# Kernel tuning notes

Hardware: AMD Instinct MI355X
Metric: run time of the kernel (lower is better)

Reference implementation:

```python
import jax, jax.numpy as jnp
import numpy as np

TAU = 1.0
TOP_K = 2
TOP_C = 8
EPS = 1e-12


def _stable_softmax(v):
    # matches torch: exp(v - max) / (sum + 1e-12)
    e = jnp.exp(v - jnp.max(v, axis=-1, keepdims=True))
    return e / (jnp.sum(e, axis=-1, keepdims=True) + EPS)


def setup_inputs() -> dict:
    key = jax.random.key(0)
    kx, kw = jax.random.split(key)
    B, D, M = 16384, 2048, 64
    x = jax.random.normal(kx, (B, D), dtype=jnp.float32)
    W = jax.random.normal(kw, (M, D), dtype=jnp.float32) * (1.0 / np.sqrt(D))
    return {"x": x, "W": W}


def reference(x, W):
    # router GEMM: [B, D] x [M, D]^T -> [B, M]
    router_logits = jnp.einsum('bd,md->bm', x, W)
    scaled_logits = router_logits / TAU
    probs = _stable_softmax(scaled_logits)
    # double top-k: first candidates (top_c), then top_k among candidates
    topc_vals, topc_idx = jax.lax.top_k(scaled_logits, TOP_C)   # [B, C]
    topk_vals, topk_pos_in_C = jax.lax.top_k(topc_vals, TOP_K)  # [B, K]
    topk_idx = jnp.take_along_axis(topc_idx, topk_pos_in_C, axis=1)
    topk_weights = _stable_softmax(topk_vals)
    return (topk_idx.astype(jnp.int64), topk_weights, probs, topc_idx.astype(jnp.int64))
```

## Files before the change

kernel.cpp:

```cpp
#include <hip/hip_runtime.h>


typedef __attribute__((ext_vector_type(8))) short short8;
typedef __attribute__((ext_vector_type(4))) float f32x4;

constexpr int Bq = 16384;
constexpr int Dk = 2048;
constexpr int Me = 64;
constexpr int WAVES = 8;
constexpr int ROWS = 32;
constexpr int KCHUNK = Dk / WAVES;
constexpr int NT = KCHUNK / 32;

constexpr size_t OFF_TOPK_IDX = 0;
constexpr size_t OFF_TOPK_W   = (size_t)Bq * 2;
constexpr size_t OFF_PROBS    = (size_t)Bq * 4;
constexpr size_t OFF_TOPC_IDX = (size_t)Bq * 4 + (size_t)Bq * 64;

__device__ __forceinline__ unsigned f2bf2(float lo, float hi) {
  unsigned r;
  asm("v_cvt_pk_bf16_f32 %0, %1, %2" : "=v"(r) : "v"(lo), "v"(hi));
  return r;
}
__device__ __forceinline__ float bflo(unsigned u) { return __builtin_bit_cast(float, u << 16); }
__device__ __forceinline__ float bfhi(unsigned u) { return __builtin_bit_cast(float, u & 0xFFFF0000u); }

__device__ __forceinline__ void split3(const float af[8], short8& s0, short8& s1, short8& s2) {
  uint4 q0, q1, q2;
  unsigned* p0 = &q0.x; unsigned* p1 = &q1.x; unsigned* p2 = &q2.x;
  #pragma unroll
  for (int p = 0; p < 4; ++p) {
    float a = af[2 * p], b = af[2 * p + 1];
    unsigned c0 = f2bf2(a, b);
    float r0a = a - bflo(c0), r0b = b - bfhi(c0);
    unsigned c1 = f2bf2(r0a, r0b);
    float r1a = r0a - bflo(c1), r1b = r0b - bfhi(c1);
    unsigned c2 = f2bf2(r1a, r1b);
    p0[p] = c0; p1[p] = c1; p2[p] = c2;
  }
  s0 = __builtin_bit_cast(short8, q0);
  s1 = __builtin_bit_cast(short8, q1);
  s2 = __builtin_bit_cast(short8, q2);
}

__global__ void wsplit_kernel(const float* __restrict__ W,
                              unsigned short* __restrict__ w0,
                              unsigned short* __restrict__ w1,
                              unsigned short* __restrict__ w2) {
  int t = blockIdx.x * blockDim.x + threadIdx.x;
  int kt = t >> 8, n = (t >> 6) & 3, L = t & 63;
  int e  = n * 16 + (L & 15);
  int kb = kt * 32 + ((L >> 4) << 3);
  const float* src = W + (size_t)e * Dk + kb;
  float4 a = *reinterpret_cast<const float4*>(src);
  float4 b = *reinterpret_cast<const float4*>(src + 4);
  float af[8] = {a.x, a.y, a.z, a.w, b.x, b.y, b.z, b.w};
  short8 s0, s1, s2;
  split3(af, s0, s1, s2);
  *reinterpret_cast<short8*>(w0 + (size_t)t * 8) = s0;
  *reinterpret_cast<short8*>(w1 + (size_t)t * 8) = s1;
  *reinterpret_cast<short8*>(w2 + (size_t)t * 8) = s2;
}

__global__ __launch_bounds__(512, 4)
void gating_mfma(const float* __restrict__ x,
                 const unsigned short* __restrict__ w0,
                 const unsigned short* __restrict__ w1,
                 const unsigned short* __restrict__ w2,
                 float* __restrict__ out) {
  __shared__ __align__(16) char smem[WAVES * ROWS * 64 * 4];
  typedef float XaT[ROWS][36];
  XaT* xa = reinterpret_cast<XaT*>(smem);
  typedef float PartT[ROWS][64];
  PartT* part = reinterpret_cast<PartT*>(smem);

  const int tid  = threadIdx.x;
  const int wv   = tid >> 6;
  const int L    = tid & 63;
  const int lidx = L & 15;
  const int kgrp = L >> 4;
  const int rowBase = blockIdx.x * ROWS;
  const int kBase = wv * KCHUNK;

  const int srow = L >> 3;
  const int sc4  = (L & 7) << 2;
  const float* xg0 = x + (size_t)(rowBase +      srow) * Dk + kBase + sc4;
  const float* xg1 = x + (size_t)(rowBase +  8 + srow) * Dk + kBase + sc4;
  const float* xg2 = x + (size_t)(rowBase + 16 + srow) * Dk + kBase + sc4;
  const float* xg3 = x + (size_t)(rowBase + 24 + srow) * Dk + kBase + sc4;

  const size_t bbase = (size_t)kBase * 64 + (size_t)L * 8;

  f32x4 acc[2][4];
  #pragma unroll
  for (int rg = 0; rg < 2; ++rg)
    #pragma unroll
    for (int n = 0; n < 4; ++n) acc[rg][n] = (f32x4){0.f, 0.f, 0.f, 0.f};

  *reinterpret_cast<float4*>(&xa[wv][     srow][sc4]) = *reinterpret_cast<const float4*>(xg0);
  *reinterpret_cast<float4*>(&xa[wv][ 8 + srow][sc4]) = *reinterpret_cast<const float4*>(xg1);
  *reinterpret_cast<float4*>(&xa[wv][16 + srow][sc4]) = *reinterpret_cast<const float4*>(xg2);
  *reinterpret_cast<float4*>(&xa[wv][24 + srow][sc4]) = *reinterpret_cast<const float4*>(xg3);

  #pragma unroll 1
  for (int kt = 0; kt < NT; ++kt) {
    float4 aLo0 = *reinterpret_cast<const float4*>(&xa[wv][     lidx][kgrp * 8]);
    float4 aHi0 = *reinterpret_cast<const float4*>(&xa[wv][     lidx][kgrp * 8 + 4]);
    float4 aLo1 = *reinterpret_cast<const float4*>(&xa[wv][16 + lidx][kgrp * 8]);
    float4 aHi1 = *reinterpret_cast<const float4*>(&xa[wv][16 + lidx][kgrp * 8 + 4]);

    float4 h0, h1, h2, h3;
    if (kt < NT - 1) {
      h0 = *reinterpret_cast<const float4*>(xg0 + (kt + 1) * 32);
      h1 = *reinterpret_cast<const float4*>(xg1 + (kt + 1) * 32);
      h2 = *reinterpret_cast<const float4*>(xg2 + (kt + 1) * 32);
      h3 = *reinterpret_cast<const float4*>(xg3 + (kt + 1) * 32);
    }

    const size_t to = bbase + (size_t)kt * 2048;

    short8 b0[4];
    #pragma unroll
    for (int n = 0; n < 4; ++n) b0[n] = *reinterpret_cast<const short8*>(w0 + to + n * 512);

    float af0[8] = {aLo0.x, aLo0.y, aLo0.z, aLo0.w, aHi0.x, aHi0.y, aHi0.z, aHi0.w};
    float af1[8] = {aLo1.x, aLo1.y, aLo1.z, aLo1.w, aHi1.x, aHi1.y, aHi1.z, aHi1.w};
    short8 xs00, xs10, xs20, xs01, xs11, xs21;
    split3(af0, xs00, xs10, xs20);
    split3(af1, xs01, xs11, xs21);

    short8 b1[4];
    #pragma unroll
    for (int n = 0; n < 4; ++n) b1[n] = *reinterpret_cast<const short8*>(w1 + to + n * 512);

    #pragma unroll
    for (int n = 0; n < 4; ++n) acc[0][n] = __builtin_amdgcn_mfma_f32_16x16x32_bf16(xs00, b0[n], acc[0][n], 0, 0, 0);
    #pragma unroll
    for (int n = 0; n < 4; ++n) acc[1][n] = __builtin_amdgcn_mfma_f32_16x16x32_bf16(xs01, b0[n], acc[1][n], 0, 0, 0);
    #pragma unroll
    for (int n = 0; n < 4; ++n) acc[0][n] = __builtin_amdgcn_mfma_f32_16x16x32_bf16(xs10, b0[n], acc[0][n], 0, 0, 0);
    #pragma unroll
    for (int n = 0; n < 4; ++n) acc[1][n] = __builtin_amdgcn_mfma_f32_16x16x32_bf16(xs11, b0[n], acc[1][n], 0, 0, 0);
    #pragma unroll
    for (int n = 0; n < 4; ++n) acc[0][n] = __builtin_amdgcn_mfma_f32_16x16x32_bf16(xs20, b0[n], acc[0][n], 0, 0, 0);
    #pragma unroll
    for (int n = 0; n < 4; ++n) acc[1][n] = __builtin_amdgcn_mfma_f32_16x16x32_bf16(xs21, b0[n], acc[1][n], 0, 0, 0);

    short8 b2[4];
    #pragma unroll
    for (int n = 0; n < 4; ++n) b2[n] = *reinterpret_cast<const short8*>(w2 + to + n * 512);

    #pragma unroll
    for (int n = 0; n < 4; ++n) acc[0][n] = __builtin_amdgcn_mfma_f32_16x16x32_bf16(xs00, b1[n], acc[0][n], 0, 0, 0);
    #pragma unroll
    for (int n = 0; n < 4; ++n) acc[1][n] = __builtin_amdgcn_mfma_f32_16x16x32_bf16(xs01, b1[n], acc[1][n], 0, 0, 0);
    #pragma unroll
    for (int n = 0; n < 4; ++n) acc[0][n] = __builtin_amdgcn_mfma_f32_16x16x32_bf16(xs10, b1[n], acc[0][n], 0, 0, 0);
    #pragma unroll
    for (int n = 0; n < 4; ++n) acc[1][n] = __builtin_amdgcn_mfma_f32_16x16x32_bf16(xs11, b1[n], acc[1][n], 0, 0, 0);

    #pragma unroll
    for (int n = 0; n < 4; ++n) acc[0][n] = __builtin_amdgcn_mfma_f32_16x16x32_bf16(xs00, b2[n], acc[0][n], 0, 0, 0);
    #pragma unroll
    for (int n = 0; n < 4; ++n) acc[1][n] = __builtin_amdgcn_mfma_f32_16x16x32_bf16(xs01, b2[n], acc[1][n], 0, 0, 0);

    if (kt < NT - 1) {
      *reinterpret_cast<float4*>(&xa[wv][     srow][sc4]) = h0;
      *reinterpret_cast<float4*>(&xa[wv][ 8 + srow][sc4]) = h1;
      *reinterpret_cast<float4*>(&xa[wv][16 + srow][sc4]) = h2;
      *reinterpret_cast<float4*>(&xa[wv][24 + srow][sc4]) = h3;
    }
  }

  __syncthreads();

  #pragma unroll
  for (int rg = 0; rg < 2; ++rg)
    #pragma unroll
    for (int n = 0; n < 4; ++n)
      #pragma unroll
      for (int r = 0; r < 4; ++r)
        part[wv][rg * 16 + kgrp * 4 + r][n * 16 + lidx] = acc[rg][n][r];
  __syncthreads();

  const int row = tid >> 4;
  const int g   = tid & 15;
  const int c4  = g * 4;
  const size_t grow = (size_t)rowBase + row;

  float4 v = {0.f, 0.f, 0.f, 0.f};
  #pragma unroll
  for (int p = 0; p < WAVES; ++p) {
    float4 t = *reinterpret_cast<const float4*>(&part[p][row][c4]);
    v.x += t.x; v.y += t.y; v.z += t.z; v.w += t.w;
  }
  float pv[4] = {v.x, v.y, v.z, v.w};

  float mx = fmaxf(fmaxf(pv[0], pv[1]), fmaxf(pv[2], pv[3]));
  #pragma unroll
  for (int m = 1; m < 16; m <<= 1) mx = fmaxf(mx, __shfl_xor(mx, m));
  float e[4], sum = 0.f;
  #pragma unroll
  for (int j = 0; j < 4; ++j) { e[j] = expf(pv[j] - mx); sum += e[j]; }
  #pragma unroll
  for (int m = 1; m < 16; m <<= 1) sum += __shfl_xor(sum, m);
  const float inv = 1.f / (sum + 1e-12f);
  float4 pw = {e[0] * inv, e[1] * inv, e[2] * inv, e[3] * inv};
  *reinterpret_cast<float4*>(out + OFF_PROBS + grow * 64 + c4) = pw;

  unsigned taken = 0;
  int bidx0 = 0, bidx1 = 0;
  float tv0 = 0.f, tv1 = 0.f;
  #pragma unroll 1
  for (int rank = 0; rank < 8; ++rank) {
    float best = -3.4e38f;
    int bl = -1;
    #pragma unroll
    for (int j = 0; j < 4; ++j)
      if (!((taken >> j) & 1u) && pv[j] > best) { best = pv[j]; bl = j; }
    int bidx = (bl >= 0) ? (c4 + bl) : (1 << 30);
    #pragma unroll
    for (int m = 1; m < 16; m <<= 1) {
      float ov = __shfl_xor(best, m);
      int   oi = __shfl_xor(bidx, m);
      if (ov > best || (ov == best && oi < bidx)) { best = ov; bidx = oi; }
    }
    if (bidx >= c4 && bidx < c4 + 4) taken |= 1u << (bidx - c4);
    if (g == 0) out[OFF_TOPC_IDX + grow * 8 + rank] = (float)bidx;
    if (rank == 0) { tv0 = best; bidx0 = bidx; }
    if (rank == 1) { tv1 = best; bidx1 = bidx; }
  }

  if (g == 0) {
    out[OFF_TOPK_IDX + grow * 2 + 0] = (float)bidx0;
    out[OFF_TOPK_IDX + grow * 2 + 1] = (float)bidx1;
    const float e1  = expf(tv1 - tv0);
    const float den = 1.f + e1 + 1e-12f;
    out[OFF_TOPK_W + grow * 2 + 0] = 1.f / den;
    out[OFF_TOPK_W + grow * 2 + 1] = e1 / den;
  }
}

extern "C" void kernel_launch(void* const* d_in, const int* in_sizes, int n_in,
                              void* d_out, int out_size, void* d_ws, size_t ws_size,
                              hipStream_t stream) {
  const float* x = (const float*)d_in[0];
  const float* W = (const float*)d_in[1];
  float* out = (float*)d_out;

  unsigned short* w0 = (unsigned short*)d_ws;
  unsigned short* w1 = w0 + (size_t)Me * Dk;
  unsigned short* w2 = w1 + (size_t)Me * Dk;

  hipLaunchKernelGGL(wsplit_kernel, dim3((Me * Dk / 8) / 256), dim3(256), 0, stream, W, w0, w1, w2);
  hipLaunchKernelGGL(gating_mfma, dim3(Bq / ROWS), dim3(512), 0, stream, x, w0, w1, w2, out);
}
```

Baseline: 46.43 us.

## Stage x tiles via direct global-to-LDS loads with double buffering and XOR swizzle

Replaces the register-staged x tile copy with __builtin_amdgcn_global_load_lds into a double-buffered per-wave LDS region. An XOR swizzle on the global column replaces the padded row layout to avoid bank conflicts. All three W split loads are also hoisted to the top of each iteration. The aim is to cut VGPR pressure and the register round trip, and to overlap the next tile's fetch with the MFMA work. The risk is correctness: the loop has no explicit vmcnt wait or barrier before reading the staged LDS, so it relies on the compiler inserting waits. Hoisting the W loads also raises live registers.

```diff
diff --git a/kernel.cpp b/kernel.cpp
--- a/kernel.cpp
+++ b/kernel.cpp
@@ -68,8 +68,8 @@
                  const unsigned short* __restrict__ w1,
                  const unsigned short* __restrict__ w2,
                  float* __restrict__ out) {
-  __shared__ __align__(16) char smem[WAVES * ROWS * 64 * 4];
-  typedef float XaT[ROWS][36];
+  __shared__ __align__(16) float smem[2 * WAVES * ROWS * 32];
+  typedef float XaT[ROWS][32];
   XaT* xa = reinterpret_cast<XaT*>(smem);
   typedef float PartT[ROWS][64];
   PartT* part = reinterpret_cast<PartT*>(smem);
@@ -83,13 +83,14 @@
   const int kBase = wv * KCHUNK;
 
   const int srow = L >> 3;
-  const int sc4  = (L & 7) << 2;
-  const float* xg0 = x + (size_t)(rowBase +      srow) * Dk + kBase + sc4;
-  const float* xg1 = x + (size_t)(rowBase +  8 + srow) * Dk + kBase + sc4;
-  const float* xg2 = x + (size_t)(rowBase + 16 + srow) * Dk + kBase + sc4;
-  const float* xg3 = x + (size_t)(rowBase + 24 + srow) * Dk + kBase + sc4;
+  const int scol = ((L & 7) ^ (srow & 7)) << 2;
+  const float* xg0 = x + (size_t)(rowBase +      srow) * Dk + kBase + scol;
+  const float* xg1 = x + (size_t)(rowBase +  8 + srow) * Dk + kBase + scol;
+  const float* xg2 = x + (size_t)(rowBase + 16 + srow) * Dk + kBase + scol;
+  const float* xg3 = x + (size_t)(rowBase + 24 + srow) * Dk + kBase + scol;
 
   const size_t bbase = (size_t)kBase * 64 + (size_t)L * 8;
+  const int s = L & 7;
 
   f32x4 acc[2][4];
   #pragma unroll
@@ -97,31 +98,46 @@
     #pragma unroll
     for (int n = 0; n < 4; ++n) acc[rg][n] = (f32x4){0.f, 0.f, 0.f, 0.f};
 
-  *reinterpret_cast<float4*>(&xa[wv][     srow][sc4]) = *reinterpret_cast<const float4*>(xg0);
-  *reinterpret_cast<float4*>(&xa[wv][ 8 + srow][sc4]) = *reinterpret_cast<const float4*>(xg1);
-  *reinterpret_cast<float4*>(&xa[wv][16 + srow][sc4]) = *reinterpret_cast<const float4*>(xg2);
-  *reinterpret_cast<float4*>(&xa[wv][24 + srow][sc4]) = *reinterpret_cast<const float4*>(xg3);
+  auto stage = [&](int buf, int kt_) {
+    float* lb = &xa[buf * WAVES + wv][0][0];
+    const int o = kt_ * 32;
+    __builtin_amdgcn_global_load_lds(
+        (const __attribute__((address_space(1))) void*)(xg0 + o),
+        (__attribute__((address_space(3))) void*)(lb),             16, 0, 0);
+    __builtin_amdgcn_global_load_lds(
+        (const __attribute__((address_space(1))) void*)(xg1 + o),
+        (__attribute__((address_space(3))) void*)(lb + 8 * 32),    16, 0, 0);
+    __builtin_amdgcn_global_load_lds(
+        (const __attribute__((address_space(1))) void*)(xg2 + o),
+        (__attribute__((address_space(3))) void*)(lb + 16 * 32),   16, 0, 0);
+    __builtin_amdgcn_global_load_lds(
+        (const __attribute__((address_space(1))) void*)(xg3 + o),
+        (__attribute__((address_space(3))) void*)(lb + 24 * 32),   16, 0, 0);
+  };
+
+  stage(0, 0);
 
   #pragma unroll 1
   for (int kt = 0; kt < NT; ++kt) {
-    float4 aLo0 = *reinterpret_cast<const float4*>(&xa[wv][     lidx][kgrp * 8]);
-    float4 aHi0 = *reinterpret_cast<const float4*>(&xa[wv][     lidx][kgrp * 8 + 4]);
-    float4 aLo1 = *reinterpret_cast<const float4*>(&xa[wv][16 + lidx][kgrp * 8]);
-    float4 aHi1 = *reinterpret_cast<const float4*>(&xa[wv][16 + lidx][kgrp * 8 + 4]);
-
-    float4 h0, h1, h2, h3;
-    if (kt < NT - 1) {
-      h0 = *reinterpret_cast<const float4*>(xg0 + (kt + 1) * 32);
-      h1 = *reinterpret_cast<const float4*>(xg1 + (kt + 1) * 32);
-      h2 = *reinterpret_cast<const float4*>(xg2 + (kt + 1) * 32);
-      h3 = *reinterpret_cast<const float4*>(xg3 + (kt + 1) * 32);
-    }
-
     const size_t to = bbase + (size_t)kt * 2048;
 
-    short8 b0[4];
+    short8 b0[4], b1[4], b2[4];
     #pragma unroll
     for (int n = 0; n < 4; ++n) b0[n] = *reinterpret_cast<const short8*>(w0 + to + n * 512);
+    #pragma unroll
+    for (int n = 0; n < 4; ++n) b1[n] = *reinterpret_cast<const short8*>(w1 + to + n * 512);
+    #pragma unroll
+    for (int n = 0; n < 4; ++n) b2[n] = *reinterpret_cast<const short8*>(w2 + to + n * 512);
+
+    if (kt + 1 < NT) stage((kt + 1) & 1, kt + 1);
+
+    const int xb = (kt & 1) * WAVES + wv;
+    const int u0 = (((2 * kgrp)     ^ s) << 2);
+    const int u1 = (((2 * kgrp + 1) ^ s) << 2);
+    float4 aLo0 = *reinterpret_cast<const float4*>(&xa[xb][     lidx][u0]);
+    float4 aHi0 = *reinterpret_cast<const float4*>(&xa[xb][     lidx][u1]);
+    float4 aLo1 = *reinterpret_cast<const float4*>(&xa[xb][16 + lidx][u0]);
+    float4 aHi1 = *reinterpret_cast<const float4*>(&xa[xb][16 + lidx][u1]);
 
     float af0[8] = {aLo0.x, aLo0.y, aLo0.z, aLo0.w, aHi0.x, aHi0.y, aHi0.z, aHi0.w};
     float af1[8] = {aLo1.x, aLo1.y, aLo1.z, aLo1.w, aHi1.x, aHi1.y, aHi1.z, aHi1.w};
@@ -129,10 +145,6 @@
     split3(af0, xs00, xs10, xs20);
     split3(af1, xs01, xs11, xs21);
 
-    short8 b1[4];
-    #pragma unroll
-    for (int n = 0; n < 4; ++n) b1[n] = *reinterpret_cast<const short8*>(w1 + to + n * 512);
-
     #pragma unroll
     for (int n = 0; n < 4; ++n) acc[0][n] = __builtin_amdgcn_mfma_f32_16x16x32_bf16(xs00, b0[n], acc[0][n], 0, 0, 0);
     #pragma unroll
@@ -146,10 +158,6 @@
     #pragma unroll
     for (int n = 0; n < 4; ++n) acc[1][n] = __builtin_amdgcn_mfma_f32_16x16x32_bf16(xs21, b0[n], acc[1][n], 0, 0, 0);
 
-    short8 b2[4];
-    #pragma unroll
-    for (int n = 0; n < 4; ++n) b2[n] = *reinterpret_cast<const short8*>(w2 + to + n * 512);
-
     #pragma unroll
     for (int n = 0; n < 4; ++n) acc[0][n] = __builtin_amdgcn_mfma_f32_16x16x32_bf16(xs00, b1[n], acc[0][n], 0, 0, 0);
     #pragma unroll
@@ -163,13 +171,6 @@
     for (int n = 0; n < 4; ++n) acc[0][n] = __builtin_amdgcn_mfma_f32_16x16x32_bf16(xs00, b2[n], acc[0][n], 0, 0, 0);
     #pragma unroll
     for (int n = 0; n < 4; ++n) acc[1][n] = __builtin_amdgcn_mfma_f32_16x16x32_bf16(xs01, b2[n], acc[1][n], 0, 0, 0);
-
-    if (kt < NT - 1) {
-      *reinterpret_cast<float4*>(&xa[wv][     srow][sc4]) = h0;
-      *reinterpret_cast<float4*>(&xa[wv][ 8 + srow][sc4]) = h1;
-      *reinterpret_cast<float4*>(&xa[wv][16 + srow][sc4]) = h2;
-      *reinterpret_cast<float4*>(&xa[wv][24 + srow][sc4]) = h3;
-    }
   }
 
   __syncthreads();
```

Result: slower. 47.45 us (+2.2%).

## Double-buffer x tile in LDS with XOR swizzle and software-pipelined bf16 split

Applied to the files above, without the earlier changes.

Restructures the per-wave K loop into a two-stage pipeline. The x tile is double-buffered in LDS with an XOR-swizzled layout, global loads run two steps ahead, and the bf16 three-way split for the next step is computed before the current step's MFMAs, with a sched_barrier separating the phases. The loop is also fully unrolled, and all weight fragments are loaded up front. The intent is to hide LDS and global latency behind MFMA work and to avoid bank conflicts, at the cost of more VGPRs, which may reduce occupancy under launch_bounds(512,4).

```diff
diff --git a/kernel.cpp b/kernel.cpp
--- a/kernel.cpp
+++ b/kernel.cpp
@@ -68,9 +68,7 @@
                  const unsigned short* __restrict__ w1,
                  const unsigned short* __restrict__ w2,
                  float* __restrict__ out) {
-  __shared__ __align__(16) char smem[WAVES * ROWS * 64 * 4];
-  typedef float XaT[ROWS][36];
-  XaT* xa = reinterpret_cast<XaT*>(smem);
+  __shared__ __align__(16) float smem[2 * WAVES * ROWS * 32];
   typedef float PartT[ROWS][64];
   PartT* part = reinterpret_cast<PartT*>(smem);
 
@@ -89,6 +87,13 @@
   const float* xg2 = x + (size_t)(rowBase + 16 + srow) * Dk + kBase + sc4;
   const float* xg3 = x + (size_t)(rowBase + 24 + srow) * Dk + kBase + sc4;
 
+  float* tile0 = smem + (size_t)wv * (ROWS * 32);
+  float* tile1 = smem + (size_t)(WAVES + wv) * (ROWS * 32);
+  const int uW = ((L & 7) ^ (srow & 7)) << 2;
+  const int s7 = lidx & 7;
+  const int uR0 = (((2 * kgrp)     ^ s7) << 2);
+  const int uR1 = (((2 * kgrp + 1) ^ s7) << 2);
+
   const size_t bbase = (size_t)kBase * 64 + (size_t)L * 8;
 
   f32x4 acc[2][4];
@@ -97,79 +102,98 @@
     #pragma unroll
     for (int n = 0; n < 4; ++n) acc[rg][n] = (f32x4){0.f, 0.f, 0.f, 0.f};
 
-  *reinterpret_cast<float4*>(&xa[wv][     srow][sc4]) = *reinterpret_cast<const float4*>(xg0);
-  *reinterpret_cast<float4*>(&xa[wv][ 8 + srow][sc4]) = *reinterpret_cast<const float4*>(xg1);
-  *reinterpret_cast<float4*>(&xa[wv][16 + srow][sc4]) = *reinterpret_cast<const float4*>(xg2);
-  *reinterpret_cast<float4*>(&xa[wv][24 + srow][sc4]) = *reinterpret_cast<const float4*>(xg3);
-
-  #pragma unroll 1
+  short8 xs[2][6];
+
+  float4 h0 = *reinterpret_cast<const float4*>(xg0);
+  float4 h1 = *reinterpret_cast<const float4*>(xg1);
+  float4 h2 = *reinterpret_cast<const float4*>(xg2);
+  float4 h3 = *reinterpret_cast<const float4*>(xg3);
+  *reinterpret_cast<float4*>(tile0 + (     srow) * 32 + uW) = h0;
+  *reinterpret_cast<float4*>(tile0 + ( 8 + srow) * 32 + uW) = h1;
+  *reinterpret_cast<float4*>(tile0 + (16 + srow) * 32 + uW) = h2;
+  *reinterpret_cast<float4*>(tile0 + (24 + srow) * 32 + uW) = h3;
+  h0 = *reinterpret_cast<const float4*>(xg0 + 32);
+  h1 = *reinterpret_cast<const float4*>(xg1 + 32);
+  h2 = *reinterpret_cast<const float4*>(xg2 + 32);
+  h3 = *reinterpret_cast<const float4*>(xg3 + 32);
+  {
+    float4 r0 = *reinterpret_cast<const float4*>(tile0 + (     lidx) * 32 + uR0);
+    float4 r1 = *reinterpret_cast<const float4*>(tile0 + (     lidx) * 32 + uR1);
+    float4 r2 = *reinterpret_cast<const float4*>(tile0 + (16 + lidx) * 32 + uR0);
+    float4 r3 = *reinterpret_cast<const float4*>(tile0 + (16 + lidx) * 32 + uR1);
+    float af0[8] = {r0.x, r0.y, r0.z, r0.w, r1.x, r1.y, r1.z, r1.w};
+    float af1[8] = {r2.x, r2.y, r2.z, r2.w, r3.x, r3.y, r3.z, r3.w};
+    split3(af0, xs[0][0], xs[0][1], xs[0][2]);
+    split3(af1, xs[0][3], xs[0][4], xs[0][5]);
+  }
+
+  #pragma unroll
   for (int kt = 0; kt < NT; ++kt) {
-    float4 aLo0 = *reinterpret_cast<const float4*>(&xa[wv][     lidx][kgrp * 8]);
-    float4 aHi0 = *reinterpret_cast<const float4*>(&xa[wv][     lidx][kgrp * 8 + 4]);
-    float4 aLo1 = *reinterpret_cast<const float4*>(&xa[wv][16 + lidx][kgrp * 8]);
-    float4 aHi1 = *reinterpret_cast<const float4*>(&xa[wv][16 + lidx][kgrp * 8 + 4]);
-
-    float4 h0, h1, h2, h3;
-    if (kt < NT - 1) {
-      h0 = *reinterpret_cast<const float4*>(xg0 + (kt + 1) * 32);
-      h1 = *reinterpret_cast<const float4*>(xg1 + (kt + 1) * 32);
-      h2 = *reinterpret_cast<const float4*>(xg2 + (kt + 1) * 32);
-      h3 = *reinterpret_cast<const float4*>(xg3 + (kt + 1) * 32);
+    const int p = kt & 1, q = p ^ 1;
+    const size_t to = bbase + (size_t)kt * 2048;
+
+    short8 b0[4], b1[4], b2[4];
+    #pragma unroll
+    for (int n = 0; n < 4; ++n) b0[n] = *reinterpret_cast<const short8*>(w0 + to + n * 512);
+    #pragma unroll
+    for (int n = 0; n < 4; ++n) b1[n] = *reinterpret_cast<const short8*>(w1 + to + n * 512);
+    #pragma unroll
+    for (int n = 0; n < 4; ++n) b2[n] = *reinterpret_cast<const short8*>(w2 + to + n * 512);
+
+    float4 r0, r1, r2, r3;
+    if (kt + 1 < NT) {
+      float* wb = ((kt + 1) & 1) ? tile1 : tile0;
+      *reinterpret_cast<float4*>(wb + (     srow) * 32 + uW) = h0;
+      *reinterpret_cast<float4*>(wb + ( 8 + srow) * 32 + uW) = h1;
+      *reinterpret_cast<float4*>(wb + (16 + srow) * 32 + uW) = h2;
+      *reinterpret_cast<float4*>(wb + (24 + srow) * 32 + uW) = h3;
+      if (kt + 2 < NT) {
+        h0 = *reinterpret_cast<const float4*>(xg0 + (kt + 2) * 32);
+        h1 = *reinterpret_cast<const float4*>(xg1 + (kt + 2) * 32);
+        h2 = *reinterpret_cast<const float4*>(xg2 + (kt + 2) * 32);
+        h3 = *reinterpret_cast<const float4*>(xg3 + (kt + 2) * 32);
+      }
+      r0 = *reinterpret_cast<const float4*>(wb + (     lidx) * 32 + uR0);
+      r1 = *reinterpret_cast<const float4*>(wb + (     lidx) * 32 + uR1);
+      r2 = *reinterpret_cast<const float4*>(wb + (16 + lidx) * 32 + uR0);
+      r3 = *reinterpret_cast<const float4*>(wb + (16 + lidx) * 32 + uR1);
     }
 
-    const size_t to = bbase + (size_t)kt * 2048;
-
-    short8 b0[4];
-    #pragma unroll
-    for (int n = 0; n < 4; ++n) b0[n] = *reinterpret_cast<const short8*>(w0 + to + n * 512);
-
-    float af0[8] = {aLo0.x, aLo0.y, aLo0.z, aLo0.w, aHi0.x, aHi0.y, aHi0.z, aHi0.w};
-    float af1[8] = {aLo1.x, aLo1.y, aLo1.z, aLo1.w, aHi1.x, aHi1.y, aHi1.z, aHi1.w};
-    short8 xs00, xs10, xs20, xs01, xs11, xs21;
-    split3(af0, xs00, xs10, xs20);
-    split3(af1, xs01, xs11, xs21);
-
-    short8 b1[4];
-    #pragma unroll
-    for (int n = 0; n < 4; ++n) b1[n] = *reinterpret_cast<const short8*>(w1 + to + n * 512);
-
-    #pragma unroll
-    for (int n = 0; n < 4; ++n) acc[0][n] = __builtin_amdgcn_mfma_f32_16x16x32_bf16(xs00, b0[n], acc[0][n], 0, 0, 0);
-    #pragma unroll
-    for (int n = 0; n < 4; ++n) acc[1][n] = __builtin_amdgcn_mfma_f32_16x16x32_bf16(xs01, b0[n], acc[1][n], 0, 0, 0);
-    #pragma unroll
-    for (int n = 0; n < 4; ++n) acc[0][n] = __builtin_amdgcn_mfma_f32_16x16x32_bf16(xs10, b0[n], acc[0][n], 0, 0, 0);
-    #pragma unroll
-    for (int n = 0; n < 4; ++n) acc[1][n] = __builtin_amdgcn_mfma_f32_16x16x32_bf16(xs11, b0[n], acc[1][n], 0, 0, 0);
-    #pragma unroll
-    for (int n = 0; n < 4; ++n) acc[0][n] = __builtin_amdgcn_mfma_f32_16x16x32_bf16(xs20, b0[n], acc[0][n], 0, 0, 0);
-    #pragma unroll
-    for (int n = 0; n < 4; ++n) acc[1][n] = __builtin_amdgcn_mfma_f32_16x16x32_bf16(xs21, b0[n], acc[1][n], 0, 0, 0);
-
-    short8 b2[4];
-    #pragma unroll
-    for (int n = 0; n < 4; ++n) b2[n] = *reinterpret_cast<const short8*>(w2 + to + n * 512);
-
-    #pragma unroll
-    for (int n = 0; n < 4; ++n) acc[0][n] = __builtin_amdgcn_mfma_f32_16x16x32_bf16(xs00, b1[n], acc[0][n], 0, 0, 0);
-    #pragma unroll
-    for (int n = 0; n < 4; ++n) acc[1][n] = __builtin_amdgcn_mfma_f32_16x16x32_bf16(xs01, b1[n], acc[1][n], 0, 0, 0);
-    #pragma unroll
-    for (int n = 0; n < 4; ++n) acc[0][n] = __builtin_amdgcn_mfma_f32_16x16x32_bf16(xs10, b1[n], acc[0][n], 0, 0, 0);
-    #pragma unroll
-    for (int n = 0; n < 4; ++n) acc[1][n] = __builtin_amdgcn_mfma_f32_16x16x32_bf16(xs11, b1[n], acc[1][n], 0, 0, 0);
-
-    #pragma unroll
-    for (int n = 0; n < 4; ++n) acc[0][n] = __builtin_amdgcn_mfma_f32_16x16x32_bf16(xs00, b2[n], acc[0][n], 0, 0, 0);
-    #pragma unroll
-    for (int n = 0; n < 4; ++n) acc[1][n] = __builtin_amdgcn_mfma_f32_16x16x32_bf16(xs01, b2[n], acc[1][n], 0, 0, 0);
-
-    if (kt < NT - 1) {
-      *reinterpret_cast<float4*>(&xa[wv][     srow][sc4]) = h0;
-      *reinterpret_cast<float4*>(&xa[wv][ 8 + srow][sc4]) = h1;
-      *reinterpret_cast<float4*>(&xa[wv][16 + srow][sc4]) = h2;
-      *reinterpret_cast<float4*>(&xa[wv][24 + srow][sc4]) = h3;
+    __builtin_amdgcn_sched_barrier(0);
+
+    if (kt + 1 < NT) {
+      float af0[8] = {r0.x, r0.y, r0.z, r0.w, r1.x, r1.y, r1.z, r1.w};
+      float af1[8] = {r2.x, r2.y, r2.z, r2.w, r3.x, r3.y, r3.z, r3.w};
+      split3(af0, xs[q][0], xs[q][1], xs[q][2]);
+      split3(af1, xs[q][3], xs[q][4], xs[q][5]);
     }
+
+    #pragma unroll
+    for (int n = 0; n < 4; ++n) acc[0][n] = __builtin_amdgcn_mfma_f32_16x16x32_bf16(xs[p][0], b0[n], acc[0][n], 0, 0, 0);
+    #pragma unroll
+    for (int n = 0; n < 4; ++n) acc[1][n] = __builtin_amdgcn_mfma_f32_16x16x32_bf16(xs[p][3], b0[n], acc[1][n], 0, 0, 0);
+    #pragma unroll
+    for (int n = 0; n < 4; ++n) acc[0][n] = __builtin_amdgcn_mfma_f32_16x16x32_bf16(xs[p][1], b0[n], acc[0][n], 0, 0, 0);
+    #pragma unroll
+    for (int n = 0; n < 4; ++n) acc[1][n] = __builtin_amdgcn_mfma_f32_16x16x32_bf16(xs[p][4], b0[n], acc[1][n], 0, 0, 0);
+    #pragma unroll
+    for (int n = 0; n < 4; ++n) acc[0][n] = __builtin_amdgcn_mfma_f32_16x16x32_bf16(xs[p][2], b0[n], acc[0][n], 0, 0, 0);
+    #pragma unroll
+    for (int n = 0; n < 4; ++n) acc[1][n] = __builtin_amdgcn_mfma_f32_16x16x32_bf16(xs[p][5], b0[n], acc[1][n], 0, 0, 0);
+
+    #pragma unroll
+    for (int n = 0; n < 4; ++n) acc[0][n] = __builtin_amdgcn_mfma_f32_16x16x32_bf16(xs[p][0], b1[n], acc[0][n], 0, 0, 0);
+    #pragma unroll
+    for (int n = 0; n < 4; ++n) acc[1][n] = __builtin_amdgcn_mfma_f32_16x16x32_bf16(xs[p][3], b1[n], acc[1][n], 0, 0, 0);
+    #pragma unroll
+    for (int n = 0; n < 4; ++n) acc[0][n] = __builtin_amdgcn_mfma_f32_16x16x32_bf16(xs[p][1], b1[n], acc[0][n], 0, 0, 0);
+    #pragma unroll
+    for (int n = 0; n < 4; ++n) acc[1][n] = __builtin_amdgcn_mfma_f32_16x16x32_bf16(xs[p][4], b1[n], acc[1][n], 0, 0, 0);
+
+    #pragma unroll
+    for (int n = 0; n < 4; ++n) acc[0][n] = __builtin_amdgcn_mfma_f32_16x16x32_bf16(xs[p][0], b2[n], acc[0][n], 0, 0, 0);
+    #pragma unroll
+    for (int n = 0; n < 4; ++n) acc[1][n] = __builtin_amdgcn_mfma_f32_16x16x32_bf16(xs[p][5 - 2], b2[n], acc[1][n], 0, 0, 0);
   }
 
   __syncthreads();
@@ -190,8 +214,8 @@
 
   float4 v = {0.f, 0.f, 0.f, 0.f};
   #pragma unroll
-  for (int p = 0; p < WAVES; ++p) {
-    float4 t = *reinterpret_cast<const float4*>(&part[p][row][c4]);
+  for (int pp = 0; pp < WAVES; ++pp) {
+    float4 t = *reinterpret_cast<const float4*>(&part[pp][row][c4]);
     v.x += t.x; v.y += t.y; v.z += t.z; v.w += t.w;
   }
   float pv[4] = {v.x, v.y, v.z, v.w};
```

New measurement: 92.09 us. +98.3%, slower.
